# Kernel optimization log

Measured on AMD Instinct MI355X. Metric: run time of the kernel, lower is better.

Reference implementation:

```python
import jax, jax.numpy as jnp
import numpy as np

N, K, D = 65536, 64, 128
ALPHA = 1.0

def setup_inputs() -> dict:
    key = jax.random.key(0)
    k1, k2 = jax.random.split(key)
    z = jax.random.normal(k1, (N, D), dtype=jnp.float32)
    centroids = jax.random.normal(k2, (K, D), dtype=jnp.float32)
    return {"z": z, "centroids": centroids}

def reference(z, centroids):
    # squared euclidean distance per (sample, cluster): sum over feature dim
    diff = jnp.sum((z[:, None, :] - centroids[None, :, :]) ** 2, axis=2)  # [N, K]
    numerator = 1.0 / (1.0 + diff / ALPHA)
    power = (ALPHA + 1.0) / 2.0
    numerator = numerator ** power
    q = numerator / jnp.sum(numerator, axis=1, keepdims=True)  # row-normalized soft assignment
    return q
```

## Files before the change

### kernel.cpp

```cpp
#include <hip/hip_runtime.h>
#include <hip/hip_bf16.h>


using bf16x8 = __attribute__((ext_vector_type(8))) __bf16;
using f32x4  = __attribute__((ext_vector_type(4))) float;

constexpr int K_CL = 64;
constexpr int D_FT = 128;

__global__ __launch_bounds__(256) void prep_kernel(
    const float* __restrict__ cent,
    __bf16* __restrict__ cb,
    float* __restrict__ bv)
{
    const int t = threadIdx.x;
    const int c = t >> 2, q = t & 3;
    const float4* p = reinterpret_cast<const float4*>(cent + c * D_FT + q * 32);
    bf16x8* dst = reinterpret_cast<bf16x8*>(cb + c * D_FT + q * 32);
    float s = 0.f;
    #pragma unroll
    for (int h = 0; h < 4; ++h) {
        float4 u = p[2 * h], v = p[2 * h + 1];
        s = fmaf(u.x, u.x, s); s = fmaf(u.y, u.y, s);
        s = fmaf(u.z, u.z, s); s = fmaf(u.w, u.w, s);
        s = fmaf(v.x, v.x, s); s = fmaf(v.y, v.y, s);
        s = fmaf(v.z, v.z, s); s = fmaf(v.w, v.w, s);
        bf16x8 a;
        a[0] = (__bf16)u.x; a[1] = (__bf16)u.y;
        a[2] = (__bf16)u.z; a[3] = (__bf16)u.w;
        a[4] = (__bf16)v.x; a[5] = (__bf16)v.y;
        a[6] = (__bf16)v.z; a[7] = (__bf16)v.w;
        dst[h] = a;
    }
    s += __shfl_xor(s, 1);
    s += __shfl_xor(s, 2);
    if (q == 0) bv[c] = 1.f + s;
}

__global__ __launch_bounds__(256) void cluster_assign_mfma(
    const float* __restrict__ z,
    const __bf16* __restrict__ cb,
    const float* __restrict__ bv,
    float* __restrict__ out)
{
    const int tid  = threadIdx.x;
    const int wave = tid >> 6;
    const int lane = tid & 63;
    const int lo   = lane & 15;
    const int g    = lane >> 4;

    const int rowbase = blockIdx.x * 64 + wave * 16;

    const char* zb = reinterpret_cast<const char*>(z)
                   + (size_t)(rowbase + lo) * 512 + g * 32;
    float4 zst[8];
    #pragma unroll
    for (int kk = 0; kk < 4; ++kk) {
        zst[2*kk]   = *reinterpret_cast<const float4*>(zb + kk * 128);
        zst[2*kk+1] = *reinterpret_cast<const float4*>(zb + kk * 128 + 16);
    }

    float bmine[4];
    #pragma unroll
    for (int nt = 0; nt < 4; ++nt) bmine[nt] = bv[lo + nt * 16];

    float zn = 0.f;
    #pragma unroll
    for (int j = 0; j < 8; ++j) {
        float4 v = zst[j];
        zn = fmaf(v.x, v.x, zn); zn = fmaf(v.y, v.y, zn);
        zn = fmaf(v.z, v.z, zn); zn = fmaf(v.w, v.w, zn);
    }
    zn += __shfl_xor(zn, 16);
    zn += __shfl_xor(zn, 32);

    bf16x8 af[4];
    #pragma unroll
    for (int kk = 0; kk < 4; ++kk) {
        float4 u = zst[2*kk], v = zst[2*kk+1];
        bf16x8 a;
        a[0] = (__bf16)u.x; a[1] = (__bf16)u.y;
        a[2] = (__bf16)u.z; a[3] = (__bf16)u.w;
        a[4] = (__bf16)v.x; a[5] = (__bf16)v.y;
        a[6] = (__bf16)v.z; a[7] = (__bf16)v.w;
        af[kk] = a;
    }

    f32x4 acc[4] = {{0,0,0,0},{0,0,0,0},{0,0,0,0},{0,0,0,0}};
    #pragma unroll
    for (int kk = 0; kk < 4; ++kk)
        #pragma unroll
        for (int nt = 0; nt < 4; ++nt) {
            bf16x8 b = *reinterpret_cast<const bf16x8*>(
                cb + (lo + nt * 16) * D_FT + kk * 32 + g * 8);
            acc[nt] = __builtin_amdgcn_mfma_f32_16x16x32_bf16(
                          af[kk], b, acc[nt], 0, 0, 0);
        }

    float znr[4];
    #pragma unroll
    for (int r = 0; r < 4; ++r) znr[r] = __shfl(zn, g * 4 + r);

    float num[4][4];
    float psum[4] = {0.f, 0.f, 0.f, 0.f};
    #pragma unroll
    for (int nt = 0; nt < 4; ++nt)
        #pragma unroll
        for (int r = 0; r < 4; ++r) {
            float d1 = fmaf(-2.f, acc[nt][r], znr[r] + bmine[nt]);
            float nv = __builtin_amdgcn_rcpf(d1);
            num[nt][r] = nv;
            psum[r] += nv;
        }
    #pragma unroll
    for (int r = 0; r < 4; ++r) {
        psum[r] += __shfl_xor(psum[r], 1);
        psum[r] += __shfl_xor(psum[r], 2);
        psum[r] += __shfl_xor(psum[r], 4);
        psum[r] += __shfl_xor(psum[r], 8);
        psum[r] = __builtin_amdgcn_rcpf(psum[r]);
    }

    #pragma unroll
    for (int nt = 0; nt < 4; ++nt)
        #pragma unroll
        for (int r = 0; r < 4; ++r)
            out[(size_t)(rowbase + g * 4 + r) * K_CL + lo + nt * 16]
                = num[nt][r] * psum[r];
}

extern "C" void kernel_launch(void* const* d_in, const int* in_sizes, int n_in,
                              void* d_out, int out_size, void* d_ws, size_t ws_size,
                              hipStream_t stream) {
    const float* z    = (const float*)d_in[0];
    const float* cent = (const float*)d_in[1];
    float* out        = (float*)d_out;

    __bf16* cb = (__bf16*)d_ws;
    float*  bv = (float*)((char*)d_ws + 16384);

    prep_kernel<<<dim3(1), dim3(256), 0, stream>>>(cent, cb, bv);
    cluster_assign_mfma<<<dim3(65536 / 64), dim3(256), 0, stream>>>(z, cb, bv, out);
}
```

Baseline: 90.64 us.

## Fuse centroid prep into main kernel via LDS and process two row tiles per block

Drops the separate single-block prep kernel. Each block now converts the centroids to bf16 in padded shared memory and computes their norms itself. B fragments are loaded once into registers and reused across two 64-row tiles, and the grid is halved to 512 blocks. This removes one launch and the serial dependency on a tiny one-block kernel. In exchange, every block redoes the centroid conversion (32KB of fp32 reads, mostly L2 hits), keeps 64 more registers live, and the launch has fewer blocks to hide latency with.

```diff
diff --git a/kernel.cpp b/kernel.cpp
--- a/kernel.cpp
+++ b/kernel.cpp
@@ -7,126 +7,133 @@
 
 constexpr int K_CL = 64;
 constexpr int D_FT = 128;
-
-__global__ __launch_bounds__(256) void prep_kernel(
-    const float* __restrict__ cent,
-    __bf16* __restrict__ cb,
-    float* __restrict__ bv)
-{
-    const int t = threadIdx.x;
-    const int c = t >> 2, q = t & 3;
-    const float4* p = reinterpret_cast<const float4*>(cent + c * D_FT + q * 32);
-    bf16x8* dst = reinterpret_cast<bf16x8*>(cb + c * D_FT + q * 32);
-    float s = 0.f;
-    #pragma unroll
-    for (int h = 0; h < 4; ++h) {
-        float4 u = p[2 * h], v = p[2 * h + 1];
-        s = fmaf(u.x, u.x, s); s = fmaf(u.y, u.y, s);
-        s = fmaf(u.z, u.z, s); s = fmaf(u.w, u.w, s);
-        s = fmaf(v.x, v.x, s); s = fmaf(v.y, v.y, s);
-        s = fmaf(v.z, v.z, s); s = fmaf(v.w, v.w, s);
-        bf16x8 a;
-        a[0] = (__bf16)u.x; a[1] = (__bf16)u.y;
-        a[2] = (__bf16)u.z; a[3] = (__bf16)u.w;
-        a[4] = (__bf16)v.x; a[5] = (__bf16)v.y;
-        a[6] = (__bf16)v.z; a[7] = (__bf16)v.w;
-        dst[h] = a;
-    }
-    s += __shfl_xor(s, 1);
-    s += __shfl_xor(s, 2);
-    if (q == 0) bv[c] = 1.f + s;
-}
+constexpr int CSTR = 136;
 
 __global__ __launch_bounds__(256) void cluster_assign_mfma(
     const float* __restrict__ z,
-    const __bf16* __restrict__ cb,
-    const float* __restrict__ bv,
+    const float* __restrict__ cent,
     float* __restrict__ out)
 {
+    __shared__ __bf16 c_bf[K_CL * CSTR];
+    __shared__ float  b_lds[K_CL];
+
     const int tid  = threadIdx.x;
     const int wave = tid >> 6;
     const int lane = tid & 63;
     const int lo   = lane & 15;
     const int g    = lane >> 4;
 
-    const int rowbase = blockIdx.x * 64 + wave * 16;
+    {
+        const int c = tid >> 2, q = tid & 3;
+        const float4* p =
+            reinterpret_cast<const float4*>(cent + c * D_FT + q * 32);
+        bf16x8* dst = reinterpret_cast<bf16x8*>(&c_bf[c * CSTR + q * 32]);
+        float s = 0.f;
+        #pragma unroll
+        for (int h = 0; h < 4; ++h) {
+            float4 u = p[2 * h], v = p[2 * h + 1];
+            s = fmaf(u.x, u.x, s); s = fmaf(u.y, u.y, s);
+            s = fmaf(u.z, u.z, s); s = fmaf(u.w, u.w, s);
+            s = fmaf(v.x, v.x, s); s = fmaf(v.y, v.y, s);
+            s = fmaf(v.z, v.z, s); s = fmaf(v.w, v.w, s);
+            bf16x8 a;
+            a[0] = (__bf16)u.x; a[1] = (__bf16)u.y;
+            a[2] = (__bf16)u.z; a[3] = (__bf16)u.w;
+            a[4] = (__bf16)v.x; a[5] = (__bf16)v.y;
+            a[6] = (__bf16)v.z; a[7] = (__bf16)v.w;
+            dst[h] = a;
+        }
+        s += __shfl_xor(s, 1);
+        s += __shfl_xor(s, 2);
+        if (q == 0) b_lds[c] = 1.f + s;
+    }
+    __syncthreads();
 
-    const char* zb = reinterpret_cast<const char*>(z)
-                   + (size_t)(rowbase + lo) * 512 + g * 32;
-    float4 zst[8];
+    bf16x8 bfr[4][4];
     #pragma unroll
-    for (int kk = 0; kk < 4; ++kk) {
-        zst[2*kk]   = *reinterpret_cast<const float4*>(zb + kk * 128);
-        zst[2*kk+1] = *reinterpret_cast<const float4*>(zb + kk * 128 + 16);
-    }
+    for (int nt = 0; nt < 4; ++nt)
+        #pragma unroll
+        for (int kk = 0; kk < 4; ++kk)
+            bfr[nt][kk] = *reinterpret_cast<const bf16x8*>(
+                &c_bf[(lo + nt * 16) * CSTR + kk * 32 + g * 8]);
 
     float bmine[4];
     #pragma unroll
-    for (int nt = 0; nt < 4; ++nt) bmine[nt] = bv[lo + nt * 16];
+    for (int nt = 0; nt < 4; ++nt) bmine[nt] = b_lds[lo + nt * 16];
 
-    float zn = 0.f;
-    #pragma unroll
-    for (int j = 0; j < 8; ++j) {
-        float4 v = zst[j];
-        zn = fmaf(v.x, v.x, zn); zn = fmaf(v.y, v.y, zn);
-        zn = fmaf(v.z, v.z, zn); zn = fmaf(v.w, v.w, zn);
-    }
-    zn += __shfl_xor(zn, 16);
-    zn += __shfl_xor(zn, 32);
+    for (int it = 0; it < 2; ++it) {
+        const int rowbase = blockIdx.x * 128 + it * 64 + wave * 16;
 
-    bf16x8 af[4];
-    #pragma unroll
-    for (int kk = 0; kk < 4; ++kk) {
-        float4 u = zst[2*kk], v = zst[2*kk+1];
-        bf16x8 a;
-        a[0] = (__bf16)u.x; a[1] = (__bf16)u.y;
-        a[2] = (__bf16)u.z; a[3] = (__bf16)u.w;
-        a[4] = (__bf16)v.x; a[5] = (__bf16)v.y;
-        a[6] = (__bf16)v.z; a[7] = (__bf16)v.w;
-        af[kk] = a;
-    }
-
-    f32x4 acc[4] = {{0,0,0,0},{0,0,0,0},{0,0,0,0},{0,0,0,0}};
-    #pragma unroll
-    for (int kk = 0; kk < 4; ++kk)
+        const char* zb = reinterpret_cast<const char*>(z)
+                       + (size_t)(rowbase + lo) * 512 + g * 32;
+        float4 zst[8];
         #pragma unroll
-        for (int nt = 0; nt < 4; ++nt) {
-            bf16x8 b = *reinterpret_cast<const bf16x8*>(
-                cb + (lo + nt * 16) * D_FT + kk * 32 + g * 8);
-            acc[nt] = __builtin_amdgcn_mfma_f32_16x16x32_bf16(
-                          af[kk], b, acc[nt], 0, 0, 0);
+        for (int kk = 0; kk < 4; ++kk) {
+            zst[2*kk]   = *reinterpret_cast<const float4*>(zb + kk * 128);
+            zst[2*kk+1] = *reinterpret_cast<const float4*>(zb + kk * 128 + 16);
         }
 
-    float znr[4];
-    #pragma unroll
-    for (int r = 0; r < 4; ++r) znr[r] = __shfl(zn, g * 4 + r);
+        float zn = 0.f;
+        #pragma unroll
+        for (int j = 0; j < 8; ++j) {
+            float4 v = zst[j];
+            zn = fmaf(v.x, v.x, zn); zn = fmaf(v.y, v.y, zn);
+            zn = fmaf(v.z, v.z, zn); zn = fmaf(v.w, v.w, zn);
+        }
+        zn += __shfl_xor(zn, 16);
+        zn += __shfl_xor(zn, 32);
 
-    float num[4][4];
-    float psum[4] = {0.f, 0.f, 0.f, 0.f};
-    #pragma unroll
-    for (int nt = 0; nt < 4; ++nt)
+        bf16x8 af[4];
+        #pragma unroll
+        for (int kk = 0; kk < 4; ++kk) {
+            float4 u = zst[2*kk], v = zst[2*kk+1];
+            bf16x8 a;
+            a[0] = (__bf16)u.x; a[1] = (__bf16)u.y;
+            a[2] = (__bf16)u.z; a[3] = (__bf16)u.w;
+            a[4] = (__bf16)v.x; a[5] = (__bf16)v.y;
+            a[6] = (__bf16)v.z; a[7] = (__bf16)v.w;
+            af[kk] = a;
+        }
+
+        f32x4 acc[4] = {{0,0,0,0},{0,0,0,0},{0,0,0,0},{0,0,0,0}};
+        #pragma unroll
+        for (int kk = 0; kk < 4; ++kk)
+            #pragma unroll
+            for (int nt = 0; nt < 4; ++nt)
+                acc[nt] = __builtin_amdgcn_mfma_f32_16x16x32_bf16(
+                              af[kk], bfr[nt][kk], acc[nt], 0, 0, 0);
+
+        float znr[4];
+        #pragma unroll
+        for (int r = 0; r < 4; ++r) znr[r] = __shfl(zn, g * 4 + r);
+
+        float num[4][4];
+        float psum[4] = {0.f, 0.f, 0.f, 0.f};
+        #pragma unroll
+        for (int nt = 0; nt < 4; ++nt)
+            #pragma unroll
+            for (int r = 0; r < 4; ++r) {
+                float d1 = fmaf(-2.f, acc[nt][r], znr[r] + bmine[nt]);
+                float nv = __builtin_amdgcn_rcpf(d1);
+                num[nt][r] = nv;
+                psum[r] += nv;
+            }
         #pragma unroll
         for (int r = 0; r < 4; ++r) {
-            float d1 = fmaf(-2.f, acc[nt][r], znr[r] + bmine[nt]);
-            float nv = __builtin_amdgcn_rcpf(d1);
-            num[nt][r] = nv;
-            psum[r] += nv;
+            psum[r] += __shfl_xor(psum[r], 1);
+            psum[r] += __shfl_xor(psum[r], 2);
+            psum[r] += __shfl_xor(psum[r], 4);
+            psum[r] += __shfl_xor(psum[r], 8);
+            psum[r] = __builtin_amdgcn_rcpf(psum[r]);
         }
-    #pragma unroll
-    for (int r = 0; r < 4; ++r) {
-        psum[r] += __shfl_xor(psum[r], 1);
-        psum[r] += __shfl_xor(psum[r], 2);
-        psum[r] += __shfl_xor(psum[r], 4);
-        psum[r] += __shfl_xor(psum[r], 8);
-        psum[r] = __builtin_amdgcn_rcpf(psum[r]);
+
+        #pragma unroll
+        for (int nt = 0; nt < 4; ++nt)
+            #pragma unroll
+            for (int r = 0; r < 4; ++r)
+                out[(size_t)(rowbase + g * 4 + r) * K_CL + lo + nt * 16]
+                    = num[nt][r] * psum[r];
     }
-
-    #pragma unroll
-    for (int nt = 0; nt < 4; ++nt)
-        #pragma unroll
-        for (int r = 0; r < 4; ++r)
-            out[(size_t)(rowbase + g * 4 + r) * K_CL + lo + nt * 16]
-                = num[nt][r] * psum[r];
 }
 
 extern "C" void kernel_launch(void* const* d_in, const int* in_sizes, int n_in,
@@ -136,9 +143,6 @@
     const float* cent = (const float*)d_in[1];
     float* out        = (float*)d_out;
 
-    __bf16* cb = (__bf16*)d_ws;
-    float*  bv = (float*)((char*)d_ws + 16384);
-
-    prep_kernel<<<dim3(1), dim3(256), 0, stream>>>(cent, cb, bv);
-    cluster_assign_mfma<<<dim3(65536 / 64), dim3(256), 0, stream>>>(z, cb, bv, out);
+    dim3 grid(65536 / 128);
+    cluster_assign_mfma<<<grid, dim3(256), 0, stream>>>(z, cent, out);
 }
```

After: 80.59 us. -11.1%, faster.
